# Optimization experiments

Measured on AMD Instinct MI355X. Metric: run time of the kernel, lower is better.

The kernel has to match this reference:

```python
import jax, jax.numpy as jnp
import numpy as np

SEQ_LEN = 12      # PRED_LEN
H_DIM = 128
EMB_DIM = 64
NPEDS = 65536


def setup_inputs() -> dict:
    key = jax.random.key(0)
    ks = jax.random.split(key, 12)
    s = 0.05
    return {
        "last_pos": jax.random.normal(ks[0], (NPEDS, 2), jnp.float32),
        "last_pos_rel": jax.random.normal(ks[1], (NPEDS, 2), jnp.float32),
        "h0": jax.random.normal(ks[2], (NPEDS, H_DIM), jnp.float32),
        "c0": jax.random.normal(ks[3], (NPEDS, H_DIM), jnp.float32),
        # LSTM params (torch gate order: i, f, g, o)
        "w_ih": jax.random.normal(ks[4], (4 * H_DIM, EMB_DIM), jnp.float32) * s,
        "w_hh": jax.random.normal(ks[5], (4 * H_DIM, H_DIM), jnp.float32) * s,
        "b_ih": jax.random.normal(ks[6], (4 * H_DIM,), jnp.float32) * s,
        "b_hh": jax.random.normal(ks[7], (4 * H_DIM,), jnp.float32) * s,
        # spatial_embedding: Linear(2, EMB_DIM)
        "w_se": jax.random.normal(ks[8], (EMB_DIM, 2), jnp.float32) * s,
        "b_se": jax.random.normal(ks[9], (EMB_DIM,), jnp.float32) * s,
        # hidden2pos: Linear(H_DIM, 2)
        "w_hp": jax.random.normal(ks[10], (2, H_DIM), jnp.float32) * s,
        "b_hp": jax.random.normal(ks[11], (2,), jnp.float32) * s,
    }


def reference(last_pos, last_pos_rel, h0, c0,
              w_ih, w_hh, b_ih, b_hh, w_se, b_se, w_hp, b_hp):
    b = b_ih + b_hh  # fold the two LSTM biases
    dec_in0 = last_pos_rel @ w_se.T + b_se          # [N, EMB]

    def step(carry, _):
        h, c, dec_in, lp = carry
        gates = dec_in @ w_ih.T + h @ w_hh.T + b    # [N, 4H]
        i, f, g, o = jnp.split(gates, 4, axis=-1)
        c = jax.nn.sigmoid(f) * c + jax.nn.sigmoid(i) * jnp.tanh(g)
        h = jax.nn.sigmoid(o) * jnp.tanh(c)
        rel = h @ w_hp.T + b_hp                     # [N, 2]
        lp = rel + lp                               # curr_pos
        dec_in = rel @ w_se.T + b_se                # next embedding input
        return (h, c, dec_in, lp), rel

    _, rels = jax.lax.scan(step, (h0, c0, dec_in0, last_pos), None, length=SEQ_LEN)
    return rels  # [SEQ_LEN, N, 2] == pred_traj_fake_rel
```

## Files before the change

### kernel.cpp

```cpp
#include <hip/hip_runtime.h>

typedef __attribute__((ext_vector_type(8))) short bf16x8;
typedef __attribute__((ext_vector_type(4))) short bf16x4;
typedef __attribute__((ext_vector_type(4))) float f32x4;

#define NPEDS 65536
#define SEQ 12
#define HD 128
#define ED 64
#define MBLK 64
#define P1 136
#define WHH_FRAGS 128
#define WEFF_FRAGS 132
#define NFRAGS (WHH_FRAGS + WEFF_FRAGS)

__device__ __forceinline__ short f2bf(float x) {
  unsigned u = __builtin_bit_cast(unsigned, x);
  u += 0x7FFFu + ((u >> 16) & 1u);
  return (short)(u >> 16);
}
__device__ __forceinline__ float sigm(float x) {
  return __builtin_amdgcn_rcpf(1.0f + __expf(-x));
}
__device__ __forceinline__ float tanh_(float x) {
  return 1.0f - 2.0f * __builtin_amdgcn_rcpf(1.0f + __expf(2.0f * x));
}

__device__ __forceinline__ int pe_grp(int a) {
  return (a >> 3) * 32 + (a & 3) * 8 + ((a >> 2) & 1) * 4;
}

__global__ void prep_kernel(const float* __restrict__ w_ih,
                            const float* __restrict__ w_hh,
                            const float* __restrict__ w_se,
                            const float* __restrict__ w_hp,
                            const float* __restrict__ b_ih,
                            const float* __restrict__ b_hh,
                            const float* __restrict__ b_se,
                            const float* __restrict__ b_hp,
                            short* __restrict__ wsB, float* __restrict__ fl) {
  int t = blockIdx.x * 256 + threadIdx.x;
  if (t < WHH_FRAGS * 64) {
    int frag = t >> 6, l = t & 63;
    int cc = frag >> 4, g = (frag >> 2) & 3, kt = frag & 3;
    int n = g * HD + cc * 16 + (l & 15);
    bf16x8 v;
#pragma unroll
    for (int e = 0; e < 8; ++e) {
      int k = kt * 32 + ((l >> 4) << 2) + (e & 3) + ((e >> 2) << 4);
      v[e] = f2bf(w_hh[n * HD + k]);
    }
    *(bf16x8*)(wsB + (size_t)frag * 512 + l * 8) = v;
  } else if (t < NFRAGS * 64) {
    int u = t - WHH_FRAGS * 64;
    int frag = u >> 6, l = u & 63;
    int llo = l & 15;
    int ks[8];
#pragma unroll
    for (int e = 0; e < 8; ++e)
      ks[e] = (frag & 3) * 32 + ((l >> 4) << 2) + (e & 3) + ((e >> 2) << 4);
    float acc[8];
    if (frag < 128) {
      int cc = frag >> 4, g = (frag >> 2) & 3;
      int n = g * HD + cc * 16 + llo;
#pragma unroll
      for (int e = 0; e < 8; ++e) acc[e] = w_hh[n * HD + ks[e]];
      for (int j = 0; j < ED; ++j) {
        float wij = w_ih[n * ED + j];
        float se0 = w_se[2 * j], se1 = w_se[2 * j + 1];
#pragma unroll
        for (int e = 0; e < 8; ++e)
          acc[e] += wij * (se0 * w_hp[ks[e]] + se1 * w_hp[HD + ks[e]]);
      }
    } else {
#pragma unroll
      for (int e = 0; e < 8; ++e)
        acc[e] = (llo < 2) ? w_hp[llo * HD + ks[e]] : 0.f;
    }
    bf16x8 v;
#pragma unroll
    for (int e = 0; e < 8; ++e) v[e] = f2bf(acc[e]);
    *(bf16x8*)(wsB + (size_t)(WHH_FRAGS + frag) * 512 + l * 8) = v;
  } else if (t < NFRAGS * 64 + 512) {
    int n = t - NFRAGS * 64;
    float b = b_ih[n] + b_hh[n];
    float s0 = 0.f, w20 = 0.f, w21 = 0.f;
    for (int j = 0; j < ED; ++j) {
      float wij = w_ih[n * ED + j];
      s0 += wij * b_se[j];
      w20 += wij * w_se[2 * j];
      w21 += wij * w_se[2 * j + 1];
    }
    fl[n] = b + s0 + w20 * b_hp[0] + w21 * b_hp[1];
    fl[512 + n] = b + s0;
    fl[1024 + 2 * n] = w20;
    fl[1024 + 2 * n + 1] = w21;
  }
}

__global__ __launch_bounds__(512, 2) void lstm_kernel(
    const float* __restrict__ lpr, const float* __restrict__ h0,
    const float* __restrict__ c0, const float* __restrict__ b_hp,
    const short* __restrict__ wsB, const float* __restrict__ fl,
    float* __restrict__ out) {
  __shared__ __align__(16) short hb[2][MBLK * P1];
  __shared__ float s_lpr[MBLK * 2];

  const int tid = threadIdx.x;
  const int cc = tid >> 6;
  const int l = tid & 63;
  const int lhi = l >> 4;
  const int llo = l & 15;
  const int p0 = blockIdx.x * MBLK;
  const int hoff = (cc >> 1) * 32 + (llo >> 2) * 8 + (cc & 1) * 4 + (llo & 3);

  if (tid < 128) s_lpr[tid] = lpr[(size_t)p0 * 2 + tid];

  float biasE[4];
#pragma unroll
  for (int g = 0; g < 4; ++g) biasE[g] = fl[g * HD + cc * 16 + llo];

  float creg[4][4];
#pragma unroll
  for (int Mt = 0; Mt < 4; ++Mt)
#pragma unroll
    for (int r = 0; r < 4; ++r)
      creg[Mt][r] =
          c0[(size_t)(p0 + Mt * 16 + lhi * 4 + r) * HD + cc * 16 + llo];

  const float bhp_l = (llo < 2) ? b_hp[llo] : 0.f;

#pragma unroll
  for (int i = 0; i < 4; ++i) {
    int grp = i * 512 + tid;
    int p = grp >> 5, a = grp & 31;
    f32x4 v = *(const f32x4*)(h0 + (size_t)(p0 + p) * HD + a * 4);
    bf16x4 s;
    s[0] = f2bf(v[0]); s[1] = f2bf(v[1]); s[2] = f2bf(v[2]); s[3] = f2bf(v[3]);
    *(bf16x4*)(&hb[0][p * P1 + pe_grp(a)]) = s;
  }
  __syncthreads();

  auto lstm_update = [&](f32x4 (&acc)[4][4], short* An) {
#pragma unroll
    for (int Mt = 0; Mt < 4; ++Mt)
#pragma unroll
      for (int r = 0; r < 4; ++r) {
        float gi = acc[0][Mt][r], gf = acc[1][Mt][r];
        float gg = acc[2][Mt][r], go = acc[3][Mt][r];
        float cn = sigm(gf) * creg[Mt][r] + sigm(gi) * tanh_(gg);
        creg[Mt][r] = cn;
        An[(Mt * 16 + lhi * 4 + r) * P1 + hoff] = f2bf(sigm(go) * tanh_(cn));
      }
  };

  auto rel_tail = [&](const short* A, int s) {
    const short* wsR = wsB + (size_t)(WHH_FRAGS + 128) * 512;
    const int Mt = cc - 4;
    f32x4 ar = {bhp_l, bhp_l, bhp_l, bhp_l};
#pragma unroll
    for (int kt = 0; kt < 4; ++kt) {
      bf16x8 Bf = *(const bf16x8*)(wsR + (size_t)kt * 512 + l * 8);
      bf16x8 Afr =
          *(const bf16x8*)(&A[(Mt * 16 + llo) * P1 + kt * 32 + lhi * 8]);
      ar = __builtin_amdgcn_mfma_f32_16x16x32_bf16(Afr, Bf, ar, 0, 0, 0);
    }
    if (llo < 2) {
#pragma unroll
      for (int r = 0; r < 4; ++r)
        out[(size_t)s * (NPEDS * 2) +
            (size_t)(p0 + Mt * 16 + lhi * 4 + r) * 2 + llo] = ar[r];
    }
  };

  {
    float b0r[4], w20r[4], w21r[4];
#pragma unroll
    for (int g = 0; g < 4; ++g) {
      int n = g * HD + cc * 16 + llo;
      b0r[g] = fl[512 + n];
      w20r[g] = fl[1024 + 2 * n];
      w21r[g] = fl[1024 + 2 * n + 1];
    }
    f32x4 acc[4][4];
#pragma unroll
    for (int g = 0; g < 4; ++g) {
      f32x4 bv = {b0r[g], b0r[g], b0r[g], b0r[g]};
#pragma unroll
      for (int Mt = 0; Mt < 4; ++Mt) acc[g][Mt] = bv;
    }
#pragma unroll
    for (int kt = 0; kt < 4; ++kt) {
      bf16x8 Af[4];
#pragma unroll
      for (int Mt = 0; Mt < 4; ++Mt)
        Af[Mt] =
            *(const bf16x8*)(&hb[0][(Mt * 16 + llo) * P1 + kt * 32 + lhi * 8]);
#pragma unroll
      for (int g = 0; g < 4; ++g) {
        bf16x8 Bf = *(const bf16x8*)(wsB +
                        (size_t)((cc * 4 + g) * 4 + kt) * 512 + l * 8);
#pragma unroll
        for (int Mt = 0; Mt < 4; ++Mt)
          acc[g][Mt] = __builtin_amdgcn_mfma_f32_16x16x32_bf16(
              Af[Mt], Bf, acc[g][Mt], 0, 0, 0);
      }
    }
#pragma unroll
    for (int Mt = 0; Mt < 4; ++Mt)
#pragma unroll
      for (int r = 0; r < 4; ++r) {
        int row = Mt * 16 + lhi * 4 + r;
        float l0 = s_lpr[row * 2], l1 = s_lpr[row * 2 + 1];
#pragma unroll
        for (int g = 0; g < 4; ++g)
          acc[g][Mt][r] += w20r[g] * l0 + w21r[g] * l1;
      }
    lstm_update(acc, hb[1]);
    __syncthreads();
  }

  const short* wsW = wsB + (size_t)WHH_FRAGS * 512;
  for (int s = 1; s < SEQ; ++s) {
    const short* A = hb[s & 1];
    short* An = hb[(s + 1) & 1];
    f32x4 acc[4][4];
#pragma unroll
    for (int g = 0; g < 4; ++g) {
      f32x4 bv = {biasE[g], biasE[g], biasE[g], biasE[g]};
#pragma unroll
      for (int Mt = 0; Mt < 4; ++Mt) acc[g][Mt] = bv;
    }
#pragma unroll
    for (int kt = 0; kt < 4; ++kt) {
      bf16x8 Af[4];
#pragma unroll
      for (int Mt = 0; Mt < 4; ++Mt)
        Af[Mt] =
            *(const bf16x8*)(&A[(Mt * 16 + llo) * P1 + kt * 32 + lhi * 8]);
#pragma unroll
      for (int g = 0; g < 4; ++g) {
        bf16x8 Bf = *(const bf16x8*)(wsW +
                        (size_t)((cc * 4 + g) * 4 + kt) * 512 + l * 8);
#pragma unroll
        for (int Mt = 0; Mt < 4; ++Mt)
          acc[g][Mt] = __builtin_amdgcn_mfma_f32_16x16x32_bf16(
              Af[Mt], Bf, acc[g][Mt], 0, 0, 0);
      }
    }
    lstm_update(acc, An);
    if (cc >= 4) rel_tail(A, s - 1);
    __syncthreads();
  }

  if (cc >= 4) rel_tail(hb[SEQ & 1], SEQ - 1);
}

extern "C" void kernel_launch(void* const* d_in, const int* in_sizes, int n_in,
                              void* d_out, int out_size, void* d_ws,
                              size_t ws_size, hipStream_t stream) {
  const float* lpr = (const float*)d_in[1];
  const float* h0 = (const float*)d_in[2];
  const float* c0 = (const float*)d_in[3];
  const float* w_ih = (const float*)d_in[4];
  const float* w_hh = (const float*)d_in[5];
  const float* b_ih = (const float*)d_in[6];
  const float* b_hh = (const float*)d_in[7];
  const float* w_se = (const float*)d_in[8];
  const float* b_se = (const float*)d_in[9];
  const float* w_hp = (const float*)d_in[10];
  const float* b_hp = (const float*)d_in[11];
  short* wsB = (short*)d_ws;
  float* fl = (float*)((char*)d_ws + (size_t)NFRAGS * 512 * sizeof(short));
  float* out = (float*)d_out;

  prep_kernel<<<67, 256, 0, stream>>>(w_ih, w_hh, w_se, w_hp, b_ih, b_hh,
                                      b_se, b_hp, wsB, fl);
  lstm_kernel<<<NPEDS / MBLK, 512, 0, stream>>>(lpr, h0, c0, b_hp, wsB, fl,
                                                out);
}
```

Before: 179.0 us.

## Halve ped tile to 32, raise occupancy, fold log2e into weights for exp2 gates

Shrinks the per-block pedestrian tile from 64 to 32 rows, halving the accumulator and cell-state register footprint, and raises launch bounds to 4 blocks per CU so more waves can hide MFMA and weight-fetch latency. The gate weights and biases are prescaled by log2(e) (twice that for the g gate) in the prep kernel, so the activations use exp2 directly. The sigmoid/tanh combination is merged algebraically to use fewer reciprocals. This trades twice as many blocks, each reloading the same B fragments from global/L2, and slightly different rounding from scaling the weights before the bf16 conversion.

```diff
diff --git a/kernel.cpp b/kernel.cpp
--- a/kernel.cpp
+++ b/kernel.cpp
@@ -8,22 +8,25 @@
 #define SEQ 12
 #define HD 128
 #define ED 64
-#define MBLK 64
+#define MBLK 32
 #define P1 136
 #define WHH_FRAGS 128
 #define WEFF_FRAGS 132
 #define NFRAGS (WHH_FRAGS + WEFF_FRAGS)
+#define L2E 1.44269504088896340736f
+#define NEG2L (-2.88539008177792681472f)
 
 __device__ __forceinline__ short f2bf(float x) {
   unsigned u = __builtin_bit_cast(unsigned, x);
   u += 0x7FFFu + ((u >> 16) & 1u);
   return (short)(u >> 16);
 }
-__device__ __forceinline__ float sigm(float x) {
-  return __builtin_amdgcn_rcpf(1.0f + __expf(-x));
-}
-__device__ __forceinline__ float tanh_(float x) {
-  return 1.0f - 2.0f * __builtin_amdgcn_rcpf(1.0f + __expf(2.0f * x));
+__device__ __forceinline__ float exp2_(float x) {
+#if __has_builtin(__builtin_amdgcn_exp2f)
+  return __builtin_amdgcn_exp2f(x);
+#else
+  return exp2f(x);
+#endif
 }
 
 __device__ __forceinline__ int pe_grp(int a) {
@@ -43,12 +46,13 @@
   if (t < WHH_FRAGS * 64) {
     int frag = t >> 6, l = t & 63;
     int cc = frag >> 4, g = (frag >> 2) & 3, kt = frag & 3;
+    float fac = (g == 2) ? 2.0f * L2E : L2E;
     int n = g * HD + cc * 16 + (l & 15);
     bf16x8 v;
 #pragma unroll
     for (int e = 0; e < 8; ++e) {
       int k = kt * 32 + ((l >> 4) << 2) + (e & 3) + ((e >> 2) << 4);
-      v[e] = f2bf(w_hh[n * HD + k]);
+      v[e] = f2bf(w_hh[n * HD + k] * fac);
     }
     *(bf16x8*)(wsB + (size_t)frag * 512 + l * 8) = v;
   } else if (t < NFRAGS * 64) {
@@ -62,6 +66,7 @@
     float acc[8];
     if (frag < 128) {
       int cc = frag >> 4, g = (frag >> 2) & 3;
+      float fac = (g == 2) ? 2.0f * L2E : L2E;
       int n = g * HD + cc * 16 + llo;
 #pragma unroll
       for (int e = 0; e < 8; ++e) acc[e] = w_hh[n * HD + ks[e]];
@@ -72,6 +77,8 @@
         for (int e = 0; e < 8; ++e)
           acc[e] += wij * (se0 * w_hp[ks[e]] + se1 * w_hp[HD + ks[e]]);
       }
+#pragma unroll
+      for (int e = 0; e < 8; ++e) acc[e] *= fac;
     } else {
 #pragma unroll
       for (int e = 0; e < 8; ++e)
@@ -83,6 +90,7 @@
     *(bf16x8*)(wsB + (size_t)(WHH_FRAGS + frag) * 512 + l * 8) = v;
   } else if (t < NFRAGS * 64 + 512) {
     int n = t - NFRAGS * 64;
+    float fac = ((n >> 7) == 2) ? 2.0f * L2E : L2E;
     float b = b_ih[n] + b_hh[n];
     float s0 = 0.f, w20 = 0.f, w21 = 0.f;
     for (int j = 0; j < ED; ++j) {
@@ -91,14 +99,14 @@
       w20 += wij * w_se[2 * j];
       w21 += wij * w_se[2 * j + 1];
     }
-    fl[n] = b + s0 + w20 * b_hp[0] + w21 * b_hp[1];
-    fl[512 + n] = b + s0;
-    fl[1024 + 2 * n] = w20;
-    fl[1024 + 2 * n + 1] = w21;
-  }
-}
-
-__global__ __launch_bounds__(512, 2) void lstm_kernel(
+    fl[n] = fac * (b + s0 + w20 * b_hp[0] + w21 * b_hp[1]);
+    fl[512 + n] = fac * (b + s0);
+    fl[1024 + 2 * n] = fac * w20;
+    fl[1024 + 2 * n + 1] = fac * w21;
+  }
+}
+
+__global__ __launch_bounds__(512, 4) void lstm_kernel(
     const float* __restrict__ lpr, const float* __restrict__ h0,
     const float* __restrict__ c0, const float* __restrict__ b_hp,
     const short* __restrict__ wsB, const float* __restrict__ fl,
@@ -114,15 +122,15 @@
   const int p0 = blockIdx.x * MBLK;
   const int hoff = (cc >> 1) * 32 + (llo >> 2) * 8 + (cc & 1) * 4 + (llo & 3);
 
-  if (tid < 128) s_lpr[tid] = lpr[(size_t)p0 * 2 + tid];
+  if (tid < 64) s_lpr[tid] = lpr[(size_t)p0 * 2 + tid];
 
   float biasE[4];
 #pragma unroll
   for (int g = 0; g < 4; ++g) biasE[g] = fl[g * HD + cc * 16 + llo];
 
-  float creg[4][4];
-#pragma unroll
-  for (int Mt = 0; Mt < 4; ++Mt)
+  float creg[2][4];
+#pragma unroll
+  for (int Mt = 0; Mt < 2; ++Mt)
 #pragma unroll
     for (int r = 0; r < 4; ++r)
       creg[Mt][r] =
@@ -131,7 +139,7 @@
   const float bhp_l = (llo < 2) ? b_hp[llo] : 0.f;
 
 #pragma unroll
-  for (int i = 0; i < 4; ++i) {
+  for (int i = 0; i < 2; ++i) {
     int grp = i * 512 + tid;
     int p = grp >> 5, a = grp & 31;
     f32x4 v = *(const f32x4*)(h0 + (size_t)(p0 + p) * HD + a * 4);
@@ -141,22 +149,30 @@
   }
   __syncthreads();
 
-  auto lstm_update = [&](f32x4 (&acc)[4][4], short* An) {
-#pragma unroll
-    for (int Mt = 0; Mt < 4; ++Mt)
+  auto lstm_update = [&](f32x4 (&acc)[4][2], short* An) {
+#pragma unroll
+    for (int Mt = 0; Mt < 2; ++Mt)
 #pragma unroll
       for (int r = 0; r < 4; ++r) {
-        float gi = acc[0][Mt][r], gf = acc[1][Mt][r];
-        float gg = acc[2][Mt][r], go = acc[3][Mt][r];
-        float cn = sigm(gf) * creg[Mt][r] + sigm(gi) * tanh_(gg);
+        float yi = acc[0][Mt][r], yf = acc[1][Mt][r];
+        float yg = acc[2][Mt][r], yo = acc[3][Mt][r];
+        float P = 1.f + exp2_(-yf);
+        float Q = 1.f + exp2_(-yi);
+        float R = 1.f + exp2_(-yg);
+        float QR = Q * R;
+        float rD = __builtin_amdgcn_rcpf(P * QR);
+        float cn = (creg[Mt][r] * QR + (2.f - R) * P) * rD;
         creg[Mt][r] = cn;
-        An[(Mt * 16 + lhi * 4 + r) * P1 + hoff] = f2bf(sigm(go) * tanh_(cn));
+        float T = 1.f + exp2_(cn * NEG2L);
+        float S = 1.f + exp2_(-yo);
+        float hn = (2.f - T) * __builtin_amdgcn_rcpf(S * T);
+        An[(Mt * 16 + lhi * 4 + r) * P1 + hoff] = f2bf(hn);
       }
   };
 
   auto rel_tail = [&](const short* A, int s) {
     const short* wsR = wsB + (size_t)(WHH_FRAGS + 128) * 512;
-    const int Mt = cc - 4;
+    const int Mt = cc - 6;
     f32x4 ar = {bhp_l, bhp_l, bhp_l, bhp_l};
 #pragma unroll
     for (int kt = 0; kt < 4; ++kt) {
@@ -174,26 +190,26 @@
   };
 
   {
-    float b0r[4], w20r[4], w21r[4];
+    f32x4 acc[4][2];
 #pragma unroll
     for (int g = 0; g < 4; ++g) {
       int n = g * HD + cc * 16 + llo;
-      b0r[g] = fl[512 + n];
-      w20r[g] = fl[1024 + 2 * n];
-      w21r[g] = fl[1024 + 2 * n + 1];
-    }
-    f32x4 acc[4][4];
-#pragma unroll
-    for (int g = 0; g < 4; ++g) {
-      f32x4 bv = {b0r[g], b0r[g], b0r[g], b0r[g]};
-#pragma unroll
-      for (int Mt = 0; Mt < 4; ++Mt) acc[g][Mt] = bv;
+      float b0 = fl[512 + n];
+      float w20 = fl[1024 + 2 * n];
+      float w21 = fl[1024 + 2 * n + 1];
+#pragma unroll
+      for (int Mt = 0; Mt < 2; ++Mt)
+#pragma unroll
+        for (int r = 0; r < 4; ++r) {
+          int row = Mt * 16 + lhi * 4 + r;
+          acc[g][Mt][r] = b0 + w20 * s_lpr[row * 2] + w21 * s_lpr[row * 2 + 1];
+        }
     }
 #pragma unroll
     for (int kt = 0; kt < 4; ++kt) {
-      bf16x8 Af[4];
-#pragma unroll
-      for (int Mt = 0; Mt < 4; ++Mt)
+      bf16x8 Af[2];
+#pragma unroll
+      for (int Mt = 0; Mt < 2; ++Mt)
         Af[Mt] =
             *(const bf16x8*)(&hb[0][(Mt * 16 + llo) * P1 + kt * 32 + lhi * 8]);
 #pragma unroll
@@ -201,21 +217,11 @@
         bf16x8 Bf = *(const bf16x8*)(wsB +
                         (size_t)((cc * 4 + g) * 4 + kt) * 512 + l * 8);
 #pragma unroll
-        for (int Mt = 0; Mt < 4; ++Mt)
+        for (int Mt = 0; Mt < 2; ++Mt)
           acc[g][Mt] = __builtin_amdgcn_mfma_f32_16x16x32_bf16(
               Af[Mt], Bf, acc[g][Mt], 0, 0, 0);
       }
     }
-#pragma unroll
-    for (int Mt = 0; Mt < 4; ++Mt)
-#pragma unroll
-      for (int r = 0; r < 4; ++r) {
-        int row = Mt * 16 + lhi * 4 + r;
-        float l0 = s_lpr[row * 2], l1 = s_lpr[row * 2 + 1];
-#pragma unroll
-        for (int g = 0; g < 4; ++g)
-          acc[g][Mt][r] += w20r[g] * l0 + w21r[g] * l1;
-      }
     lstm_update(acc, hb[1]);
     __syncthreads();
   }
@@ -224,18 +230,18 @@
   for (int s = 1; s < SEQ; ++s) {
     const short* A = hb[s & 1];
     short* An = hb[(s + 1) & 1];
-    f32x4 acc[4][4];
+    f32x4 acc[4][2];
 #pragma unroll
     for (int g = 0; g < 4; ++g) {
       f32x4 bv = {biasE[g], biasE[g], biasE[g], biasE[g]};
 #pragma unroll
-      for (int Mt = 0; Mt < 4; ++Mt) acc[g][Mt] = bv;
+      for (int Mt = 0; Mt < 2; ++Mt) acc[g][Mt] = bv;
     }
 #pragma unroll
     for (int kt = 0; kt < 4; ++kt) {
-      bf16x8 Af[4];
-#pragma unroll
-      for (int Mt = 0; Mt < 4; ++Mt)
+      bf16x8 Af[2];
+#pragma unroll
+      for (int Mt = 0; Mt < 2; ++Mt)
         Af[Mt] =
             *(const bf16x8*)(&A[(Mt * 16 + llo) * P1 + kt * 32 + lhi * 8]);
 #pragma unroll
@@ -243,17 +249,17 @@
         bf16x8 Bf = *(const bf16x8*)(wsW +
                         (size_t)((cc * 4 + g) * 4 + kt) * 512 + l * 8);
 #pragma unroll
-        for (int Mt = 0; Mt < 4; ++Mt)
+        for (int Mt = 0; Mt < 2; ++Mt)
           acc[g][Mt] = __builtin_amdgcn_mfma_f32_16x16x32_bf16(
               Af[Mt], Bf, acc[g][Mt], 0, 0, 0);
       }
     }
     lstm_update(acc, An);
-    if (cc >= 4) rel_tail(A, s - 1);
+    if (cc >= 6) rel_tail(A, s - 1);
     __syncthreads();
   }
 
-  if (cc >= 4) rel_tail(hb[SEQ & 1], SEQ - 1);
+  if (cc >= 6) rel_tail(hb[SEQ & 1], SEQ - 1);
 }
 
 extern "C" void kernel_launch(void* const* d_in, const int* in_sizes, int n_in,
```

Result: slower. 615.2 us (+243.6%).
